# Kernel optimization log

Hardware: AMD Instinct MI355X
Metric: run time of the kernel (lower is better)

The kernel has to match this reference:

```python
import jax, jax.numpy as jnp
import numpy as np
from jax import lax

N_POINTS = 4_194_304
HIDDEN = 16
N_HIDDEN_LAYERS = 8   # num_layers=9 -> 1 input layer + 8 bias-free hidden layers


def setup_inputs() -> dict:
    key = jax.random.key(0)
    k_x, k_win, k_bin, k_wh, k_wout = jax.random.split(key, 5)
    x = jax.random.uniform(k_x, (N_POINTS, 2), dtype=jnp.float32)
    # PyTorch Linear default init: U(-1/sqrt(fan_in), 1/sqrt(fan_in))
    s_in = 1.0 / np.sqrt(2.0)
    s_h = 1.0 / np.sqrt(HIDDEN)
    W_in = jax.random.uniform(k_win, (HIDDEN, 2), jnp.float32, -s_in, s_in)
    b_in = jax.random.uniform(k_bin, (HIDDEN,), jnp.float32, -s_in, s_in)
    W_hidden = jax.random.uniform(k_wh, (N_HIDDEN_LAYERS, HIDDEN, HIDDEN), jnp.float32, -s_h, s_h)
    W_out = jax.random.uniform(k_wout, (3, HIDDEN), jnp.float32, -s_h, s_h)
    return {"x": x, "W_in": W_in, "b_in": b_in, "W_hidden": W_hidden, "W_out": W_out}


def reference(x, W_in, b_in, W_hidden, W_out):
    # [N,2] -> [N,16], biased input layer + tanh
    h = jnp.tanh(x @ W_in.T + b_in)
    # 8 bias-free 16x16 layers, each followed by tanh
    def step(h, W):
        return jnp.tanh(h @ W.T), None
    h, _ = lax.scan(step, h, W_hidden)
    # output layer 16 -> 3, sigmoid to map to [0,1] RGB
    return jax.nn.sigmoid(h @ W_out.T)
```

## Files before the change

kernel.cpp:

```cpp
#include <hip/hip_runtime.h>


typedef float  f32x4 __attribute__((ext_vector_type(4)));
typedef __fp16 f16x4 __attribute__((ext_vector_type(4)));
typedef __fp16 f16x2 __attribute__((ext_vector_type(2)));

#define K2   2.8853900817779268f
#define KOUT (-1.4426950408889634f)

__device__ __forceinline__ f16x4 v4s(f32x4 y) {
    float e0 = __builtin_amdgcn_exp2f(y[0]);
    float e1 = __builtin_amdgcn_exp2f(y[1]);
    float e2 = __builtin_amdgcn_exp2f(y[2]);
    float e3 = __builtin_amdgcn_exp2f(y[3]);
    float d0 = e0 + 1.0f, d1 = e1 + 1.0f, d2 = e2 + 1.0f, d3 = e3 + 1.0f;
    float p01 = d0 * d1, p23 = d2 * d3;
    float r   = __builtin_amdgcn_rcpf(p01 * p23);
    float i01 = r * p23, i23 = r * p01;
    float v0 = i01 * d1, v1 = i01 * d0;
    float v2 = i23 * d3, v3 = i23 * d2;
    f16x2 lo = __builtin_amdgcn_cvt_pkrtz(v0, v1);
    f16x2 hi = __builtin_amdgcn_cvt_pkrtz(v2, v3);
    return __builtin_shufflevector(lo, hi, 0, 1, 2, 3);
}

__global__ __launch_bounds__(256, 6)
void artnet_kernel(const float2* __restrict__ x,
                   const float2* __restrict__ Win,
                   const float*  __restrict__ bin,
                   const float4* __restrict__ Wh,
                   const float4* __restrict__ Wout,
                   float* __restrict__ out,
                   int nPairs, int nWaves)
{
    const int tid  = blockIdx.x * 256 + threadIdx.x;
    const int gw   = tid >> 6;
    const int lane = threadIdx.x & 63;
    const int row  = lane & 15;
    const int quad = lane >> 4;

    f16x4 aw[8];
    f32x4 crs[8];
#pragma unroll
    for (int l = 0; l < 8; ++l) {
        float4 w = Wh[l * 64 + row * 4 + quad];
        const float s = -2.0f * K2;
        f16x2 lo = __builtin_amdgcn_cvt_pkrtz(w.x * s, w.y * s);
        f16x2 hi = __builtin_amdgcn_cvt_pkrtz(w.z * s, w.w * s);
        aw[l] = __builtin_shufflevector(lo, hi, 0, 1, 2, 3);
        float partial = w.x + w.y + w.z + w.w;
        partial += __shfl_xor(partial, 16, 64);
        partial += __shfl_xor(partial, 32, 64);
        f32x4 c;
#pragma unroll
        for (int i = 0; i < 4; ++i)
            c[i] = K2 * __shfl(partial, quad * 4 + i, 64);
        crs[l] = c;
    }

    f16x4 awin = {(__fp16)0.0f, (__fp16)0.0f, (__fp16)0.0f, (__fp16)0.0f};
    if (quad == 0) {
        float2 wr = Win[row];
        f16x2 lo = __builtin_amdgcn_cvt_pkrtz(wr.x * K2, wr.y * K2);
        f16x2 hi = __builtin_amdgcn_cvt_pkrtz(bin[row] * K2, 0.0f);
        awin = __builtin_shufflevector(lo, hi, 0, 1, 2, 3);
    }

    f16x4 awo = {(__fp16)0.0f, (__fp16)0.0f, (__fp16)0.0f, (__fp16)0.0f};
    float prt = 0.0f;
    if (row < 3) {
        float4 w = Wout[row * 4 + quad];
        const float s = -2.0f * KOUT;
        f16x2 lo = __builtin_amdgcn_cvt_pkrtz(w.x * s, w.y * s);
        f16x2 hi = __builtin_amdgcn_cvt_pkrtz(w.z * s, w.w * s);
        awo = __builtin_shufflevector(lo, hi, 0, 1, 2, 3);
        prt = w.x + w.y + w.z + w.w;
    }
    prt += __shfl_xor(prt, 16, 64);
    prt += __shfl_xor(prt, 32, 64);
    f32x4 crso;
#pragma unroll
    for (int i = 0; i < 4; ++i)
        crso[i] = KOUT * __shfl(prt, quad * 4 + i, 64);

    const f32x4 zero4 = {0.0f, 0.0f, 0.0f, 0.0f};
    const f16x2 one0  = {(__fp16)1.0f, (__fp16)0.0f};

    for (int pi = gw; pi < nPairs; pi += nWaves) {
        const int t0 = pi * 2;
        f16x4 bf[2];
        f32x4 acco[2];

#pragma unroll
        for (int s = 0; s < 2; ++s) {
            float2 xv = x[(t0 + s) * 16 + row];
            f16x2 lo = __builtin_amdgcn_cvt_pkrtz(xv.x, xv.y);
            bf[s] = __builtin_shufflevector(lo, one0, 0, 1, 2, 3);
        }
#pragma unroll
        for (int s = 0; s < 2; ++s) {
            f32x4 acc = __builtin_amdgcn_mfma_f32_16x16x16f16(awin, bf[s], zero4, 0, 0, 0);
            bf[s] = v4s(acc);
        }

#pragma unroll
        for (int l = 0; l < 8; ++l) {
#pragma unroll
            for (int s = 0; s < 2; ++s) {
                f32x4 acc = __builtin_amdgcn_mfma_f32_16x16x16f16(aw[l], bf[s], crs[l], 0, 0, 0);
                bf[s] = v4s(acc);
            }
        }

#pragma unroll
        for (int s = 0; s < 2; ++s)
            acco[s] = __builtin_amdgcn_mfma_f32_16x16x16f16(awo, bf[s], crso, 0, 0, 0);

        if (quad == 0) {
            float ea0 = __builtin_amdgcn_exp2f(acco[0][0]);
            float ea1 = __builtin_amdgcn_exp2f(acco[0][1]);
            float ea2 = __builtin_amdgcn_exp2f(acco[0][2]);
            float eb0 = __builtin_amdgcn_exp2f(acco[1][0]);
            float eb1 = __builtin_amdgcn_exp2f(acco[1][1]);
            float eb2 = __builtin_amdgcn_exp2f(acco[1][2]);
            float da0 = ea0 + 1.0f, da1 = ea1 + 1.0f, da2 = ea2 + 1.0f;
            float db0 = eb0 + 1.0f, db1 = eb1 + 1.0f, db2 = eb2 + 1.0f;
            float pa01 = da0 * da1, P3a = pa01 * da2;
            float pb01 = db0 * db1, P3b = pb01 * db2;
            float r  = __builtin_amdgcn_rcpf(P3a * P3b);
            float rA = r * P3b, rB = r * P3a;
            float sa2 = rA * pa01;
            float ia  = rA * da2;
            float sa0 = ia * da1, sa1 = ia * da0;
            float sb2 = rB * pb01;
            float ib  = rB * db2;
            float sb0 = ib * db1, sb1 = ib * db0;
            const int p0 = t0 * 16 + row;
            out[p0 * 3 + 0] = sa0;
            out[p0 * 3 + 1] = sa1;
            out[p0 * 3 + 2] = sa2;
            const int p1 = p0 + 16;
            out[p1 * 3 + 0] = sb0;
            out[p1 * 3 + 1] = sb1;
            out[p1 * 3 + 2] = sb2;
        }
    }
}

extern "C" void kernel_launch(void* const* d_in, const int* in_sizes, int n_in,
                              void* d_out, int out_size, void* d_ws, size_t ws_size,
                              hipStream_t stream) {
    const float2* x    = (const float2*)d_in[0];
    const float2* Win  = (const float2*)d_in[1];
    const float*  bin  = (const float*) d_in[2];
    const float4* Wh   = (const float4*)d_in[3];
    const float4* Wout = (const float4*)d_in[4];
    float* out = (float*)d_out;

    const int n      = in_sizes[0] / 2;
    const int nPairs = n / 32;
    const int blocks = 4096;
    const int nWaves = blocks * 4;

    artnet_kernel<<<blocks, 256, 0, stream>>>(x, Win, bin, Wh, Wout, out, nPairs, nWaves);
}
```

Measured before the change: 195.4 us.

## Replace exp-based sigmoid-form tanh with packed fp16 Pade rational approximation

Each tanh was computed through a sigmoid reformulation with exp2 and folded weight/bias constants. It is now a [5/4]-style Pade rational polynomial evaluated in packed fp16 math, with one shared reciprocal per four values. This drops the transcendental exp calls and the per-layer bias accumulators (crs/crso), and raises launch bounds occupancy from 6 to 8. The Pade form loses accuracy and is not clamped for large inputs, and the fp16 polynomial adds rounding error.

```diff
diff --git a/kernel.cpp b/kernel.cpp
--- a/kernel.cpp
+++ b/kernel.cpp
@@ -5,26 +5,50 @@
 typedef __fp16 f16x4 __attribute__((ext_vector_type(4)));
 typedef __fp16 f16x2 __attribute__((ext_vector_type(2)));
 
-#define K2   2.8853900817779268f
 #define KOUT (-1.4426950408889634f)
 
-__device__ __forceinline__ f16x4 v4s(f32x4 y) {
-    float e0 = __builtin_amdgcn_exp2f(y[0]);
-    float e1 = __builtin_amdgcn_exp2f(y[1]);
-    float e2 = __builtin_amdgcn_exp2f(y[2]);
-    float e3 = __builtin_amdgcn_exp2f(y[3]);
-    float d0 = e0 + 1.0f, d1 = e1 + 1.0f, d2 = e2 + 1.0f, d3 = e3 + 1.0f;
-    float p01 = d0 * d1, p23 = d2 * d3;
-    float r   = __builtin_amdgcn_rcpf(p01 * p23);
-    float i01 = r * p23, i23 = r * p01;
+__device__ __forceinline__ f16x2 splat2(float v) {
+    __fp16 h = (__fp16)v;
+    f16x2 r = {h, h};
+    return r;
+}
+
+__device__ __forceinline__ f16x4 pk_tanh4(f32x4 y) {
+    const f16x2 A1 = splat2(0.11111111f);
+    const f16x2 A2 = splat2(0.00103704f);
+    const f16x2 B1 = splat2(0.44444444f);
+    const f16x2 B2 = splat2(0.01587302f);
+    const f16x2 ONE = splat2(1.0f);
+
+    f16x2 z01 = __builtin_amdgcn_cvt_pkrtz(y[0], y[1]);
+    f16x2 z23 = __builtin_amdgcn_cvt_pkrtz(y[2], y[3]);
+    f16x2 u01 = z01 * z01;
+    f16x2 u23 = z23 * z23;
+    f16x2 p01 = __builtin_elementwise_fma(u01, A2, A1);
+    f16x2 p23 = __builtin_elementwise_fma(u23, A2, A1);
+    p01 = __builtin_elementwise_fma(u01, p01, ONE);
+    p23 = __builtin_elementwise_fma(u23, p23, ONE);
+    f16x2 n01 = z01 * p01;
+    f16x2 n23 = z23 * p23;
+    f16x2 q01 = __builtin_elementwise_fma(u01, B2, B1);
+    f16x2 q23 = __builtin_elementwise_fma(u23, B2, B1);
+    q01 = __builtin_elementwise_fma(u01, q01, ONE);
+    q23 = __builtin_elementwise_fma(u23, q23, ONE);
+    float d0 = (float)q01.x, d1 = (float)q01.y;
+    float d2 = (float)q23.x, d3 = (float)q23.y;
+    float m01 = d0 * d1, m23 = d2 * d3;
+    float r   = __builtin_amdgcn_rcpf(m01 * m23);
+    float i01 = r * m23, i23 = r * m01;
     float v0 = i01 * d1, v1 = i01 * d0;
     float v2 = i23 * d3, v3 = i23 * d2;
-    f16x2 lo = __builtin_amdgcn_cvt_pkrtz(v0, v1);
-    f16x2 hi = __builtin_amdgcn_cvt_pkrtz(v2, v3);
-    return __builtin_shufflevector(lo, hi, 0, 1, 2, 3);
+    f16x2 inv01 = __builtin_amdgcn_cvt_pkrtz(v0, v1);
+    f16x2 inv23 = __builtin_amdgcn_cvt_pkrtz(v2, v3);
+    f16x2 t01 = n01 * inv01;
+    f16x2 t23 = n23 * inv23;
+    return __builtin_shufflevector(t01, t23, 0, 1, 2, 3);
 }
 
-__global__ __launch_bounds__(256, 6)
+__global__ __launch_bounds__(256, 8)
 void artnet_kernel(const float2* __restrict__ x,
                    const float2* __restrict__ Win,
                    const float*  __restrict__ bin,
@@ -40,48 +64,29 @@
     const int quad = lane >> 4;
 
     f16x4 aw[8];
-    f32x4 crs[8];
 #pragma unroll
     for (int l = 0; l < 8; ++l) {
         float4 w = Wh[l * 64 + row * 4 + quad];
-        const float s = -2.0f * K2;
-        f16x2 lo = __builtin_amdgcn_cvt_pkrtz(w.x * s, w.y * s);
-        f16x2 hi = __builtin_amdgcn_cvt_pkrtz(w.z * s, w.w * s);
+        f16x2 lo = __builtin_amdgcn_cvt_pkrtz(w.x, w.y);
+        f16x2 hi = __builtin_amdgcn_cvt_pkrtz(w.z, w.w);
         aw[l] = __builtin_shufflevector(lo, hi, 0, 1, 2, 3);
-        float partial = w.x + w.y + w.z + w.w;
-        partial += __shfl_xor(partial, 16, 64);
-        partial += __shfl_xor(partial, 32, 64);
-        f32x4 c;
-#pragma unroll
-        for (int i = 0; i < 4; ++i)
-            c[i] = K2 * __shfl(partial, quad * 4 + i, 64);
-        crs[l] = c;
     }
 
     f16x4 awin = {(__fp16)0.0f, (__fp16)0.0f, (__fp16)0.0f, (__fp16)0.0f};
     if (quad == 0) {
         float2 wr = Win[row];
-        f16x2 lo = __builtin_amdgcn_cvt_pkrtz(wr.x * K2, wr.y * K2);
-        f16x2 hi = __builtin_amdgcn_cvt_pkrtz(bin[row] * K2, 0.0f);
+        f16x2 lo = __builtin_amdgcn_cvt_pkrtz(wr.x, wr.y);
+        f16x2 hi = __builtin_amdgcn_cvt_pkrtz(bin[row], 0.0f);
         awin = __builtin_shufflevector(lo, hi, 0, 1, 2, 3);
     }
 
     f16x4 awo = {(__fp16)0.0f, (__fp16)0.0f, (__fp16)0.0f, (__fp16)0.0f};
-    float prt = 0.0f;
     if (row < 3) {
         float4 w = Wout[row * 4 + quad];
-        const float s = -2.0f * KOUT;
-        f16x2 lo = __builtin_amdgcn_cvt_pkrtz(w.x * s, w.y * s);
-        f16x2 hi = __builtin_amdgcn_cvt_pkrtz(w.z * s, w.w * s);
+        f16x2 lo = __builtin_amdgcn_cvt_pkrtz(w.x * KOUT, w.y * KOUT);
+        f16x2 hi = __builtin_amdgcn_cvt_pkrtz(w.z * KOUT, w.w * KOUT);
         awo = __builtin_shufflevector(lo, hi, 0, 1, 2, 3);
-        prt = w.x + w.y + w.z + w.w;
     }
-    prt += __shfl_xor(prt, 16, 64);
-    prt += __shfl_xor(prt, 32, 64);
-    f32x4 crso;
-#pragma unroll
-    for (int i = 0; i < 4; ++i)
-        crso[i] = KOUT * __shfl(prt, quad * 4 + i, 64);
 
     const f32x4 zero4 = {0.0f, 0.0f, 0.0f, 0.0f};
     const f16x2 one0  = {(__fp16)1.0f, (__fp16)0.0f};
@@ -100,21 +105,21 @@
 #pragma unroll
         for (int s = 0; s < 2; ++s) {
             f32x4 acc = __builtin_amdgcn_mfma_f32_16x16x16f16(awin, bf[s], zero4, 0, 0, 0);
-            bf[s] = v4s(acc);
+            bf[s] = pk_tanh4(acc);
         }
 
 #pragma unroll
         for (int l = 0; l < 8; ++l) {
 #pragma unroll
             for (int s = 0; s < 2; ++s) {
-                f32x4 acc = __builtin_amdgcn_mfma_f32_16x16x16f16(aw[l], bf[s], crs[l], 0, 0, 0);
-                bf[s] = v4s(acc);
+                f32x4 acc = __builtin_amdgcn_mfma_f32_16x16x16f16(aw[l], bf[s], zero4, 0, 0, 0);
+                bf[s] = pk_tanh4(acc);
             }
         }
 
 #pragma unroll
         for (int s = 0; s < 2; ++s)
-            acco[s] = __builtin_amdgcn_mfma_f32_16x16x16f16(awo, bf[s], crso, 0, 0, 0);
+            acco[s] = __builtin_amdgcn_mfma_f32_16x16x16f16(awo, bf[s], zero4, 0, 0, 0);
 
         if (quad == 0) {
             float ea0 = __builtin_amdgcn_exp2f(acco[0][0]);
```

New measurement: 227.6 us. 1.16x slower.

## Process four 16-point tiles per wave and share one reciprocal across eight tanh

Applied to the files above, without the earlier changes.

Each wave now handles four tiles per iteration instead of two. Four independent MFMAs are issued per layer, so there is more instruction-level parallelism to hide MFMA latency. The tanh helper now merges eight values under a single reciprocal, replacing two reciprocals with one plus a few extra multiplies. The launch-bounds occupancy hint rises from 6 to 8 blocks per CU, which may force tighter register allocation while the per-wave working set grows, risking spills. The product of eight (1+e) terms can overflow in fp32 more easily, which risks NaN or zero for large pre-activations.

```diff
diff --git a/kernel.cpp b/kernel.cpp
--- a/kernel.cpp
+++ b/kernel.cpp
@@ -8,30 +8,43 @@
 #define K2   2.8853900817779268f
 #define KOUT (-1.4426950408889634f)
 
-__device__ __forceinline__ f16x4 v4s(f32x4 y) {
-    float e0 = __builtin_amdgcn_exp2f(y[0]);
-    float e1 = __builtin_amdgcn_exp2f(y[1]);
-    float e2 = __builtin_amdgcn_exp2f(y[2]);
-    float e3 = __builtin_amdgcn_exp2f(y[3]);
+__device__ __forceinline__ void v8s(f32x4 ya, f32x4 yb, f16x4* oa, f16x4* ob) {
+    float e0 = __builtin_amdgcn_exp2f(ya[0]);
+    float e1 = __builtin_amdgcn_exp2f(ya[1]);
+    float e2 = __builtin_amdgcn_exp2f(ya[2]);
+    float e3 = __builtin_amdgcn_exp2f(ya[3]);
+    float e4 = __builtin_amdgcn_exp2f(yb[0]);
+    float e5 = __builtin_amdgcn_exp2f(yb[1]);
+    float e6 = __builtin_amdgcn_exp2f(yb[2]);
+    float e7 = __builtin_amdgcn_exp2f(yb[3]);
     float d0 = e0 + 1.0f, d1 = e1 + 1.0f, d2 = e2 + 1.0f, d3 = e3 + 1.0f;
-    float p01 = d0 * d1, p23 = d2 * d3;
-    float r   = __builtin_amdgcn_rcpf(p01 * p23);
-    float i01 = r * p23, i23 = r * p01;
+    float d4 = e4 + 1.0f, d5 = e5 + 1.0f, d6 = e6 + 1.0f, d7 = e7 + 1.0f;
+    float m01 = d0 * d1, m23 = d2 * d3, m45 = d4 * d5, m67 = d6 * d7;
+    float mA = m01 * m23, mB = m45 * m67;
+    float r  = __builtin_amdgcn_rcpf(mA * mB);
+    float iA = r * mB, iB = r * mA;
+    float i01 = iA * m23, i23 = iA * m01;
+    float i45 = iB * m67, i67 = iB * m45;
     float v0 = i01 * d1, v1 = i01 * d0;
     float v2 = i23 * d3, v3 = i23 * d2;
-    f16x2 lo = __builtin_amdgcn_cvt_pkrtz(v0, v1);
-    f16x2 hi = __builtin_amdgcn_cvt_pkrtz(v2, v3);
-    return __builtin_shufflevector(lo, hi, 0, 1, 2, 3);
+    float v4 = i45 * d5, v5 = i45 * d4;
+    float v6 = i67 * d7, v7 = i67 * d6;
+    f16x2 a01 = __builtin_amdgcn_cvt_pkrtz(v0, v1);
+    f16x2 a23 = __builtin_amdgcn_cvt_pkrtz(v2, v3);
+    f16x2 b01 = __builtin_amdgcn_cvt_pkrtz(v4, v5);
+    f16x2 b23 = __builtin_amdgcn_cvt_pkrtz(v6, v7);
+    *oa = __builtin_shufflevector(a01, a23, 0, 1, 2, 3);
+    *ob = __builtin_shufflevector(b01, b23, 0, 1, 2, 3);
 }
 
-__global__ __launch_bounds__(256, 6)
+__global__ __launch_bounds__(256, 8)
 void artnet_kernel(const float2* __restrict__ x,
                    const float2* __restrict__ Win,
                    const float*  __restrict__ bin,
                    const float4* __restrict__ Wh,
                    const float4* __restrict__ Wout,
                    float* __restrict__ out,
-                   int nPairs, int nWaves)
+                   int nQuads, int nWaves)
 {
     const int tid  = blockIdx.x * 256 + threadIdx.x;
     const int gw   = tid >> 6;
@@ -86,63 +99,72 @@
     const f32x4 zero4 = {0.0f, 0.0f, 0.0f, 0.0f};
     const f16x2 one0  = {(__fp16)1.0f, (__fp16)0.0f};
 
-    for (int pi = gw; pi < nPairs; pi += nWaves) {
-        const int t0 = pi * 2;
-        f16x4 bf[2];
-        f32x4 acco[2];
+    for (int pi = gw; pi < nQuads; pi += nWaves) {
+        const int t0 = pi * 4;
+        f16x4 bf[4];
+        f32x4 acco[4];
 
 #pragma unroll
-        for (int s = 0; s < 2; ++s) {
+        for (int s = 0; s < 4; ++s) {
             float2 xv = x[(t0 + s) * 16 + row];
             f16x2 lo = __builtin_amdgcn_cvt_pkrtz(xv.x, xv.y);
             bf[s] = __builtin_shufflevector(lo, one0, 0, 1, 2, 3);
         }
-#pragma unroll
-        for (int s = 0; s < 2; ++s) {
-            f32x4 acc = __builtin_amdgcn_mfma_f32_16x16x16f16(awin, bf[s], zero4, 0, 0, 0);
-            bf[s] = v4s(acc);
+        {
+            f32x4 a0 = __builtin_amdgcn_mfma_f32_16x16x16f16(awin, bf[0], zero4, 0, 0, 0);
+            f32x4 a1 = __builtin_amdgcn_mfma_f32_16x16x16f16(awin, bf[1], zero4, 0, 0, 0);
+            f32x4 a2 = __builtin_amdgcn_mfma_f32_16x16x16f16(awin, bf[2], zero4, 0, 0, 0);
+            f32x4 a3 = __builtin_amdgcn_mfma_f32_16x16x16f16(awin, bf[3], zero4, 0, 0, 0);
+            v8s(a0, a1, &bf[0], &bf[1]);
+            v8s(a2, a3, &bf[2], &bf[3]);
         }
 
 #pragma unroll
         for (int l = 0; l < 8; ++l) {
-#pragma unroll
-            for (int s = 0; s < 2; ++s) {
-                f32x4 acc = __builtin_amdgcn_mfma_f32_16x16x16f16(aw[l], bf[s], crs[l], 0, 0, 0);
-                bf[s] = v4s(acc);
-            }
+            f32x4 a0 = __builtin_amdgcn_mfma_f32_16x16x16f16(aw[l], bf[0], crs[l], 0, 0, 0);
+            f32x4 a1 = __builtin_amdgcn_mfma_f32_16x16x16f16(aw[l], bf[1], crs[l], 0, 0, 0);
+            f32x4 a2 = __builtin_amdgcn_mfma_f32_16x16x16f16(aw[l], bf[2], crs[l], 0, 0, 0);
+            f32x4 a3 = __builtin_amdgcn_mfma_f32_16x16x16f16(aw[l], bf[3], crs[l], 0, 0, 0);
+            v8s(a0, a1, &bf[0], &bf[1]);
+            v8s(a2, a3, &bf[2], &bf[3]);
         }
 
 #pragma unroll
-        for (int s = 0; s < 2; ++s)
+        for (int s = 0; s < 4; ++s)
             acco[s] = __builtin_amdgcn_mfma_f32_16x16x16f16(awo, bf[s], crso, 0, 0, 0);
 
         if (quad == 0) {
-            float ea0 = __builtin_amdgcn_exp2f(acco[0][0]);
-            float ea1 = __builtin_amdgcn_exp2f(acco[0][1]);
-            float ea2 = __builtin_amdgcn_exp2f(acco[0][2]);
-            float eb0 = __builtin_amdgcn_exp2f(acco[1][0]);
-            float eb1 = __builtin_amdgcn_exp2f(acco[1][1]);
-            float eb2 = __builtin_amdgcn_exp2f(acco[1][2]);
-            float da0 = ea0 + 1.0f, da1 = ea1 + 1.0f, da2 = ea2 + 1.0f;
-            float db0 = eb0 + 1.0f, db1 = eb1 + 1.0f, db2 = eb2 + 1.0f;
-            float pa01 = da0 * da1, P3a = pa01 * da2;
-            float pb01 = db0 * db1, P3b = pb01 * db2;
-            float r  = __builtin_amdgcn_rcpf(P3a * P3b);
-            float rA = r * P3b, rB = r * P3a;
-            float sa2 = rA * pa01;
-            float ia  = rA * da2;
-            float sa0 = ia * da1, sa1 = ia * da0;
-            float sb2 = rB * pb01;
-            float ib  = rB * db2;
-            float sb0 = ib * db1, sb1 = ib * db0;
-            const int p0 = t0 * 16 + row;
-            out[p0 * 3 + 0] = sa0;
-            out[p0 * 3 + 1] = sa1;
-            out[p0 * 3 + 2] = sa2;
-            const int p1 = p0 + 16;
-            out[p1 * 3 + 0] = sb0;
-            out[p1 * 3 + 1] = sb1;
-            out[p1 * 3 + 2] = sb2;
+#pragma unroll
+            for (int g = 0; g < 2; ++g) {
+                f32x4 A = acco[g * 2 + 0];
+                f32x4 B = acco[g * 2 + 1];
+                float ea0 = __builtin_amdgcn_exp2f(A[0]);
+                float ea1 = __builtin_amdgcn_exp2f(A[1]);
+                float ea2 = __builtin_amdgcn_exp2f(A[2]);
+                float eb0 = __builtin_amdgcn_exp2f(B[0]);
+                float eb1 = __builtin_amdgcn_exp2f(B[1]);
+                float eb2 = __builtin_amdgcn_exp2f(B[2]);
+                float da0 = ea0 + 1.0f, da1 = ea1 + 1.0f, da2 = ea2 + 1.0f;
+                float db0 = eb0 + 1.0f, db1 = eb1 + 1.0f, db2 = eb2 + 1.0f;
+                float pa01 = da0 * da1, P3a = pa01 * da2;
+                float pb01 = db0 * db1, P3b = pb01 * db2;
+                float r  = __builtin_amdgcn_rcpf(P3a * P3b);
+                float rA = r * P3b, rB = r * P3a;
+                float sa2 = rA * pa01;
+                float ia  = rA * da2;
+                float sa0 = ia * da1, sa1 = ia * da0;
+                float sb2 = rB * pb01;
+                float ib  = rB * db2;
+                float sb0 = ib * db1, sb1 = ib * db0;
+                const int p0 = (t0 + g * 2) * 16 + row;
+                out[p0 * 3 + 0] = sa0;
+                out[p0 * 3 + 1] = sa1;
+                out[p0 * 3 + 2] = sa2;
+                const int p1 = p0 + 16;
+                out[p1 * 3 + 0] = sb0;
+                out[p1 * 3 + 1] = sb1;
+                out[p1 * 3 + 2] = sb2;
+            }
         }
     }
 }
@@ -158,9 +180,9 @@
     float* out = (float*)d_out;
 
     const int n      = in_sizes[0] / 2;
-    const int nPairs = n / 32;
+    const int nQuads = n / 64;
     const int blocks = 4096;
     const int nWaves = blocks * 4;
 
-    artnet_kernel<<<blocks, 256, 0, stream>>>(x, Win, bin, Wh, Wout, out, nPairs, nWaves);
+    artnet_kernel<<<blocks, 256, 0, stream>>>(x, Win, bin, Wh, Wout, out, nQuads, nWaves);
 }
```

Measured after the change: 247.4 us. +26.6%, slower.
